# Kernel tuning notes

Measured on AMD Instinct MI355X. Metric: run time of the kernel, lower is better.

Reference implementation:

```python
import jax, jax.numpy as jnp
import numpy as np

B, T, F = 1024, 256, 64
H1, H2, H3 = 64, 32, 16


def _lstm_params(key, in_dim, units, scale=0.1):
    k1, k2, k3 = jax.random.split(key, 3)
    W = jax.random.normal(k1, (in_dim, 4 * units), jnp.float32) * scale
    U = jax.random.normal(k2, (units, 4 * units), jnp.float32) * scale
    b = jax.random.normal(k3, (4 * units,), jnp.float32) * scale
    return W, U, b


def lstm_seq(x, W, U, b, reverse):
    """Keras-style LSTM (gate order i,f,g,o). Returns (all_h [B,T,H] time-aligned, last_h [B,H])."""
    Bx = x.shape[0]
    H = U.shape[0]
    xz = jnp.einsum('bti,ij->btj', x, W) + b  # [B,T,4H]
    if reverse:
        xz = xz[:, ::-1]
    xz = jnp.swapaxes(xz, 0, 1)  # [T,B,4H]

    def step(carry, zx):
        h, c = carry
        z = zx + h @ U
        i, f, g, o = jnp.split(z, 4, axis=-1)
        i = jax.nn.sigmoid(i)
        f = jax.nn.sigmoid(f)
        g = jnp.tanh(g)
        o = jax.nn.sigmoid(o)
        c = f * c + i * g
        h = o * jnp.tanh(c)
        return (h, c), h

    h0 = jnp.zeros((Bx, H), x.dtype)
    (hT, _), hs = jax.lax.scan(step, (h0, h0), xz)
    hs = jnp.swapaxes(hs, 0, 1)  # [B,T,H]
    if reverse:
        hs = hs[:, ::-1]  # Keras Bidirectional re-reverses backward outputs
    return hs, hT


def setup_inputs() -> dict:
    key = jax.random.key(0)
    ks = jax.random.split(key, 10)
    x = jax.random.normal(ks[0], (B, T, F), jnp.float32)
    W1f, U1f, b1f = _lstm_params(ks[1], F, H1)
    W1b, U1b, b1b = _lstm_params(ks[2], F, H1)
    W2f, U2f, b2f = _lstm_params(ks[3], 2 * H1, H2)
    W2b, U2b, b2b = _lstm_params(ks[4], 2 * H1, H2)
    W3f, U3f, b3f = _lstm_params(ks[5], 2 * H2, H3)
    W3b, U3b, b3b = _lstm_params(ks[6], 2 * H2, H3)
    Wd1 = jax.random.normal(ks[7], (2 * H3, 16), jnp.float32) * 0.1
    bd1 = jnp.zeros((16,), jnp.float32)
    Wd2 = jax.random.normal(ks[8], (16, 2), jnp.float32) * 0.1
    bd2 = jnp.zeros((2,), jnp.float32)
    return dict(inputs=x,
                W1f=W1f, U1f=U1f, b1f=b1f, W1b=W1b, U1b=U1b, b1b=b1b,
                W2f=W2f, U2f=U2f, b2f=b2f, W2b=W2b, U2b=U2b, b2b=b2b,
                W3f=W3f, U3f=U3f, b3f=b3f, W3b=W3b, U3b=U3b, b3b=b3b,
                Wd1=Wd1, bd1=bd1, Wd2=Wd2, bd2=bd2)


def reference(inputs,
              W1f, U1f, b1f, W1b, U1b, b1b,
              W2f, U2f, b2f, W2b, U2b, b2b,
              W3f, U3f, b3f, W3b, U3b, b3b,
              Wd1, bd1, Wd2, bd2):
    # inference path: all dropout / GaussianDropout layers are identity
    hf, _ = lstm_seq(inputs, W1f, U1f, b1f, reverse=False)
    hb, _ = lstm_seq(inputs, W1b, U1b, b1b, reverse=True)
    x = jnp.concatenate([hf, hb], axis=-1)  # [B,T,128]

    hf, _ = lstm_seq(x, W2f, U2f, b2f, reverse=False)
    hb, _ = lstm_seq(x, W2b, U2b, b2b, reverse=True)
    x = jnp.concatenate([hf, hb], axis=-1)  # [B,T,64]

    _, hf_last = lstm_seq(x, W3f, U3f, b3f, reverse=False)
    _, hb_last = lstm_seq(x, W3b, U3b, b3b, reverse=True)
    x = jnp.concatenate([hf_last, hb_last], axis=-1)  # [B,32] (Flatten is identity)

    x = jnp.clip(x @ Wd1 + bd1, 0.0, 6.0)  # relu6
    logits = x @ Wd2 + bd2
    return jax.nn.softmax(logits, axis=-1)
```

## Files before the change

kernel.cpp:

```cpp
#include <hip/hip_runtime.h>
#include <hip/hip_bf16.h>

#define T_SEQ 256
#define BATCH 1024

typedef __attribute__((ext_vector_type(8))) short  short8;
typedef __attribute__((ext_vector_type(4))) float  floatx4;
typedef unsigned short ushort_t;
typedef unsigned int   uint_t;

template <int P> struct IC { static constexpr int v = P; };

constexpr float NL2E = -1.4426950408889634f;
constexpr float L2E2 =  2.8853900817779268f;

__device__ __forceinline__ float exp2_fast(float x) {
    float r; asm("v_exp_f32 %0, %1" : "=v"(r) : "v"(x)); return r;
}
__device__ __forceinline__ float rcp_fast(float x) {
    float r; asm("v_rcp_f32 %0, %1" : "=v"(r) : "v"(x)); return r;
}
__device__ __forceinline__ ushort_t f2bf(float f) {
    union { float f; uint_t u; } v; v.f = f;
    uint_t r = v.u + 0x7FFFu + ((v.u >> 16) & 1u);
    return (ushort_t)(r >> 16);
}
__device__ __forceinline__ uint_t pk_bf16(float a, float b) {
    union { __hip_bfloat162 h; uint_t u; } v;
    v.h = __float22bfloat162_rn(make_float2(a, b));
    return v.u;
}
__device__ __forceinline__ void sync_lds() {
    asm volatile("s_waitcnt lgkmcnt(0)\n\ts_barrier" ::: "memory");
}

template <int D, int H, bool IS_FIRST, bool SEQ_OUT>
__global__ __launch_bounds__(64 * (H / 16), 1) void lstm_fused(
    const void* __restrict__ xin,
    const float* __restrict__ Wf, const float* __restrict__ Uf, const float* __restrict__ bgf,
    const float* __restrict__ Wb, const float* __restrict__ Ub, const float* __restrict__ bgb,
    void* __restrict__ outp)
{
    constexpr int UG  = H / 16;
    constexpr int KSx = D / 32;
    constexpr int KSh = (H + 31) / 32;
    constexpr int KS  = KSx + KSh;
    constexpr int HP  = (H < 32 ? 32 : H) + 8;
    constexpr int G4  = 4 * H;
    constexpr int NTH = 64 * UG;
    static_assert(D % 32 == 0 && T_SEQ % 4 == 0, "shape");

    const int tid  = threadIdx.x;
    const int ug   = tid >> 6;
    const int lane = tid & 63;
    const int lm   = lane & 15;
    const int lq   = lane >> 4;
    const int dir  = blockIdx.y;
    const int b0   = blockIdx.x * 16;

    const float* W  = dir ? Wb  : Wf;
    const float* U  = dir ? Ub  : Uf;
    const float* bg = dir ? bgb : bgf;

    __shared__ __align__(16) ushort_t hbuf[2][16][HP];

    short8 bw[4][KS];
    float  bb[4];
#pragma unroll
    for (int g = 0; g < 4; g++) {
        const float sc = (g == 2) ? L2E2 : NL2E;
        const int n = g * H + ug * 16 + lm;
        bb[g] = sc * bg[n];
#pragma unroll
        for (int ks = 0; ks < KS; ks++) {
            short8 f;
#pragma unroll
            for (int e = 0; e < 8; e++) {
                const int k = ks * 32 + lq * 8 + e;
                float v = 0.0f;
                if (k < D)          v = W[k * G4 + n];
                else if (k < D + H) v = U[(k - D) * G4 + n];
                f[e] = (short)f2bf(sc * v);
            }
            bw[g][ks] = f;
        }
    }

    for (int idx = tid; idx < 2 * 16 * HP; idx += NTH)
        ((ushort_t*)hbuf)[idx] = 0;

    float cst[4] = {0.f, 0.f, 0.f, 0.f};
    float hl[4]  = {0.f, 0.f, 0.f, 0.f};

    const int t0 = dir ? T_SEQ - 1 : 0;
    const float*    pxf = (const float*)xin + ((size_t)(b0 + lm) * T_SEQ + t0) * D + lq * 8;
    const ushort_t* pxb = (const ushort_t*)xin + ((size_t)t0 * BATCH + b0 + lm) * D + lq * 8;
    const long xstepf = dir ? -(long)D : (long)D;
    const long xstepb = (dir ? -(long)BATCH : (long)BATCH) * D;
    ushort_t* pout = (ushort_t*)outp +
        ((size_t)t0 * BATCH + b0 + lq * 4) * (2 * H) + dir * H + ug * 16 + lm;
    const long ostep = (dir ? -(long)BATCH : (long)BATCH) * (2 * H);

    float4 rawf[4][2 * KSx];
    short8 rawb[4][KSx];

    auto load_slot = [&](auto sl_) {
        constexpr int SL = decltype(sl_)::v;
        if (IS_FIRST) {
#pragma unroll
            for (int ks = 0; ks < KSx; ks++) {
                rawf[SL][2 * ks + 0] = *(const float4*)(pxf + ks * 32 + 0);
                rawf[SL][2 * ks + 1] = *(const float4*)(pxf + ks * 32 + 4);
            }
            pxf += xstepf;
        } else {
#pragma unroll
            for (int ks = 0; ks < KSx; ks++)
                rawb[SL][ks] = *(const short8*)(pxb + ks * 32);
            pxb += xstepb;
        }
    };

    load_slot(IC<0>{}); load_slot(IC<1>{}); load_slot(IC<2>{}); load_slot(IC<3>{});
    __syncthreads();

    auto step = [&](auto p_, auto sl_, int s) {
        constexpr int P  = decltype(p_)::v;
        constexpr int SL = decltype(sl_)::v;

        short8 fh[KSh];
#pragma unroll
        for (int ks = 0; ks < KSh; ks++)
            fh[ks] = *(const short8*)&hbuf[P][lm][ks * 32 + lq * 8];

        floatx4 acc[4];
#pragma unroll
        for (int g = 0; g < 4; g++) acc[g] = (floatx4){bb[g], bb[g], bb[g], bb[g]};

        short8 av[KSx];
        if (IS_FIRST) {
#pragma unroll
            for (int ks = 0; ks < KSx; ks++) {
                union { short8 s; uint_t u[4]; } f;
                const float* ra = (const float*)&rawf[SL][2 * ks];
#pragma unroll
                for (int e = 0; e < 4; e++) f.u[e] = pk_bf16(ra[2 * e], ra[2 * e + 1]);
                av[ks] = f.s;
            }
        } else {
#pragma unroll
            for (int ks = 0; ks < KSx; ks++) av[ks] = rawb[SL][ks];
        }

#pragma unroll
        for (int ks = 0; ks < KSx; ks++)
#pragma unroll
            for (int g = 0; g < 4; g++)
                acc[g] = __builtin_amdgcn_mfma_f32_16x16x32_bf16(av[ks], bw[g][ks], acc[g], 0, 0, 0);

        if (s + 4 < T_SEQ) load_slot(sl_);

#pragma unroll
        for (int ks = 0; ks < KSh; ks++)
#pragma unroll
            for (int g = 0; g < 4; g++)
                acc[g] = __builtin_amdgcn_mfma_f32_16x16x32_bf16(fh[ks], bw[g][KSx + ks], acc[g], 0, 0, 0);

#pragma unroll
        for (int r = 0; r < 4; r++) {
            const float gi = rcp_fast(1.0f + exp2_fast(acc[0][r]));
            const float gf = rcp_fast(1.0f + exp2_fast(acc[1][r]));
            const float gg = 1.0f - 2.0f * rcp_fast(1.0f + exp2_fast(acc[2][r]));
            const float go = rcp_fast(1.0f + exp2_fast(acc[3][r]));
            cst[r] = fmaf(gf, cst[r], gi * gg);
            const float tc = 1.0f - 2.0f * rcp_fast(1.0f + exp2_fast(L2E2 * cst[r]));
            const float h = go * tc;
            hl[r] = h;
            const ushort_t hw = f2bf(h);
            hbuf[P ^ 1][lq * 4 + r][ug * 16 + lm] = hw;
            if (SEQ_OUT) pout[r * 2 * H] = hw;
        }
        pout += ostep;
        if (UG > 1) sync_lds();
    };

    for (int s = 0; s < T_SEQ; s += 4) {
        step(IC<0>{}, IC<0>{}, s);
        step(IC<1>{}, IC<1>{}, s + 1);
        step(IC<0>{}, IC<2>{}, s + 2);
        step(IC<1>{}, IC<3>{}, s + 3);
    }

    if (!SEQ_OUT) {
        float* op = (float*)outp;
#pragma unroll
        for (int r = 0; r < 4; r++)
            op[(size_t)(b0 + lq * 4 + r) * (2 * H) + dir * H + ug * 16 + lm] = hl[r];
    }
}

__global__ __launch_bounds__(256) void dense_head(
    const float* __restrict__ h3, const float* __restrict__ Wd1, const float* __restrict__ bd1,
    const float* __restrict__ Wd2, const float* __restrict__ bd2, float* __restrict__ out)
{
    const int b = blockIdx.x * blockDim.x + threadIdx.x;
    if (b >= BATCH) return;
    float x[32];
#pragma unroll
    for (int k = 0; k < 32; k++) x[k] = h3[b * 32 + k];
    float y[16];
#pragma unroll
    for (int jj = 0; jj < 16; jj++) {
        float a = bd1[jj];
#pragma unroll
        for (int k = 0; k < 32; k++) a = fmaf(x[k], Wd1[k * 16 + jj], a);
        y[jj] = fminf(fmaxf(a, 0.0f), 6.0f);
    }
    float l0 = bd2[0], l1 = bd2[1];
#pragma unroll
    for (int k = 0; k < 16; k++) {
        l0 = fmaf(y[k], Wd2[k * 2 + 0], l0);
        l1 = fmaf(y[k], Wd2[k * 2 + 1], l1);
    }
    const float m = fmaxf(l0, l1);
    const float e0 = __expf(l0 - m), e1 = __expf(l1 - m);
    const float inv = 1.0f / (e0 + e1);
    out[b * 2 + 0] = e0 * inv;
    out[b * 2 + 1] = e1 * inv;
}

extern "C" void kernel_launch(void* const* d_in, const int* in_sizes, int n_in,
                              void* d_out, int out_size, void* d_ws, size_t ws_size,
                              hipStream_t stream)
{
    const float* x   = (const float*)d_in[0];
    const float* W1f = (const float*)d_in[1];
    const float* U1f = (const float*)d_in[2];
    const float* b1f = (const float*)d_in[3];
    const float* W1b = (const float*)d_in[4];
    const float* U1b = (const float*)d_in[5];
    const float* b1b = (const float*)d_in[6];
    const float* W2f = (const float*)d_in[7];
    const float* U2f = (const float*)d_in[8];
    const float* b2f = (const float*)d_in[9];
    const float* W2b = (const float*)d_in[10];
    const float* U2b = (const float*)d_in[11];
    const float* b2b = (const float*)d_in[12];
    const float* W3f = (const float*)d_in[13];
    const float* U3f = (const float*)d_in[14];
    const float* b3f = (const float*)d_in[15];
    const float* W3b = (const float*)d_in[16];
    const float* U3b = (const float*)d_in[17];
    const float* b3b = (const float*)d_in[18];
    const float* Wd1 = (const float*)d_in[19];
    const float* bd1 = (const float*)d_in[20];
    const float* Wd2 = (const float*)d_in[21];
    const float* bd2 = (const float*)d_in[22];

    char* ws = (char*)d_ws;
    void*  l1out = (void*)ws;
    void*  l2out = (void*)(ws + (size_t)64 * 1024 * 1024);
    float* h3    = (float*)(ws + (size_t)96 * 1024 * 1024);
    float* out   = (float*)d_out;

    dim3 grid(BATCH / 16, 2);

    lstm_fused<64, 64, true, true>
        <<<grid, 256, 0, stream>>>(x, W1f, U1f, b1f, W1b, U1b, b1b, l1out);
    lstm_fused<128, 32, false, true>
        <<<grid, 128, 0, stream>>>(l1out, W2f, U2f, b2f, W2b, U2b, b2b, l2out);
    lstm_fused<64, 16, false, false>
        <<<grid, 64, 0, stream>>>(l2out, W3f, U3f, b3f, W3b, U3b, b3b, h3);
    dense_head<<<dim3(BATCH / 256), 256, 0, stream>>>(h3, Wd1, bd1, Wd2, bd2, out);
}
```

Measured before the change: 517.7 us.

## Transpose LSTM MFMA so hidden state stays in registers for small layers

Swaps the MFMA operand order so gate outputs come out batch-by-unit transposed, and each lane's output fragment matches the B-operand layout of a 16x16x16 MFMA. For layers 2 and 3 a single wave now computes all hidden units and feeds h back through registers, with no LDS round trip and no barrier per timestep. Output writes also become packed 8-byte stores, and the L2E2 scale is folded into the cell state. The cost is that one wave per block does the work of two for layer 2, which lengthens each step's serial MFMA chain and raises register pressure.

```diff
diff --git a/kernel.cpp b/kernel.cpp
--- a/kernel.cpp
+++ b/kernel.cpp
@@ -5,6 +5,7 @@
 #define BATCH 1024
 
 typedef __attribute__((ext_vector_type(8))) short  short8;
+typedef __attribute__((ext_vector_type(4))) short  short4v;
 typedef __attribute__((ext_vector_type(4))) float  floatx4;
 typedef unsigned short ushort_t;
 typedef unsigned int   uint_t;
@@ -33,18 +34,28 @@
 __device__ __forceinline__ void sync_lds() {
     asm volatile("s_waitcnt lgkmcnt(0)\n\ts_barrier" ::: "memory");
 }
-
-template <int D, int H, bool IS_FIRST, bool SEQ_OUT>
-__global__ __launch_bounds__(64 * (H / 16), 1) void lstm_fused(
+__device__ __forceinline__ floatx4 mfma16(short4v a, short4v b, floatx4 c) {
+#if __has_builtin(__builtin_amdgcn_mfma_f32_16x16x16bf16_1k)
+    return __builtin_amdgcn_mfma_f32_16x16x16bf16_1k(a, b, c, 0, 0, 0);
+#else
+    floatx4 d;
+    asm("v_mfma_f32_16x16x16_bf16 %0, %1, %2, %3" : "=v"(d) : "v"(a), "v"(b), "v"(c));
+    return d;
+#endif
+}
+
+template <int D, int H, bool IS_FIRST, bool SEQ_OUT, bool REGH>
+__global__ __launch_bounds__(REGH ? 64 : 64 * (H / 16), 1) void lstm_fused(
     const void* __restrict__ xin,
     const float* __restrict__ Wf, const float* __restrict__ Uf, const float* __restrict__ bgf,
     const float* __restrict__ Wb, const float* __restrict__ Ub, const float* __restrict__ bgb,
     void* __restrict__ outp)
 {
-    constexpr int UG  = H / 16;
+    constexpr int UG  = REGH ? 1 : H / 16;
+    constexpr int NT  = REGH ? H / 16 : 1;
     constexpr int KSx = D / 32;
-    constexpr int KSh = (H + 31) / 32;
-    constexpr int KS  = KSx + KSh;
+    constexpr int KSh = REGH ? 1 : H / 32;
+    constexpr int NC  = REGH ? H / 16 : 1;
     constexpr int HP  = (H < 32 ? 32 : H) + 8;
     constexpr int G4  = 4 * H;
     constexpr int NTH = 64 * UG;
@@ -62,35 +73,71 @@
     const float* U  = dir ? Ub  : Uf;
     const float* bg = dir ? bgb : bgf;
 
-    __shared__ __align__(16) ushort_t hbuf[2][16][HP];
-
-    short8 bw[4][KS];
-    float  bb[4];
+    __shared__ __align__(16) ushort_t hbuf[REGH ? 8 : 2 * 16 * HP];
+
+    short8  aw[4][NT][KSx];
+    short8  hw[4][NT][KSh];
+    short4v uw[4][NT][NC];
+    floatx4 bias4[4][NT];
 #pragma unroll
     for (int g = 0; g < 4; g++) {
         const float sc = (g == 2) ? L2E2 : NL2E;
-        const int n = g * H + ug * 16 + lm;
-        bb[g] = sc * bg[n];
-#pragma unroll
-        for (int ks = 0; ks < KS; ks++) {
-            short8 f;
-#pragma unroll
-            for (int e = 0; e < 8; e++) {
-                const int k = ks * 32 + lq * 8 + e;
-                float v = 0.0f;
-                if (k < D)          v = W[k * G4 + n];
-                else if (k < D + H) v = U[(k - D) * G4 + n];
-                f[e] = (short)f2bf(sc * v);
-            }
-            bw[g][ks] = f;
-        }
-    }
-
-    for (int idx = tid; idx < 2 * 16 * HP; idx += NTH)
-        ((ushort_t*)hbuf)[idx] = 0;
-
-    float cst[4] = {0.f, 0.f, 0.f, 0.f};
-    float hl[4]  = {0.f, 0.f, 0.f, 0.f};
+#pragma unroll
+        for (int t = 0; t < NT; t++) {
+            const int ub = g * H + (REGH ? t * 16 : ug * 16);
+            floatx4 b4;
+#pragma unroll
+            for (int r = 0; r < 4; r++) b4[r] = sc * bg[ub + lq * 4 + r];
+            bias4[g][t] = b4;
+            const int nc = ub + lm;
+#pragma unroll
+            for (int ks = 0; ks < KSx; ks++) {
+                short8 f;
+#pragma unroll
+                for (int e = 0; e < 8; e++)
+                    f[e] = (short)f2bf(sc * W[(ks * 32 + lq * 8 + e) * G4 + nc]);
+                aw[g][t][ks] = f;
+            }
+            if constexpr (!REGH) {
+#pragma unroll
+                for (int ks = 0; ks < KSh; ks++) {
+                    short8 f;
+#pragma unroll
+                    for (int e = 0; e < 8; e++) {
+                        const int k = ks * 32 + lq * 8 + e;
+                        f[e] = (k < H) ? (short)f2bf(sc * U[k * G4 + nc]) : (short)0;
+                    }
+                    hw[g][t][ks] = f;
+                }
+            } else {
+#pragma unroll
+                for (int c = 0; c < NC; c++) {
+                    short4v f;
+#pragma unroll
+                    for (int e = 0; e < 4; e++)
+                        f[e] = (short)f2bf(sc * U[(c * 16 + lq * 4 + e) * G4 + nc]);
+                    uw[g][t][c] = f;
+                }
+            }
+        }
+    }
+
+    if constexpr (!REGH) {
+        for (int idx = tid; idx < 2 * 16 * HP; idx += NTH)
+            hbuf[idx] = 0;
+    }
+
+    float   cst[NT][4];
+    float   hl[NT][4];
+    short4v hfrag[NC];
+#pragma unroll
+    for (int t = 0; t < NT; t++)
+#pragma unroll
+        for (int r = 0; r < 4; r++) { cst[t][r] = 0.f; hl[t][r] = 0.f; }
+    if constexpr (REGH) {
+#pragma unroll
+        for (int c = 0; c < NC; c++) hfrag[c] = (short4v){0, 0, 0, 0};
+    }
 
     const int t0 = dir ? T_SEQ - 1 : 0;
     const float*    pxf = (const float*)xin + ((size_t)(b0 + lm) * T_SEQ + t0) * D + lq * 8;
@@ -98,7 +145,7 @@
     const long xstepf = dir ? -(long)D : (long)D;
     const long xstepb = (dir ? -(long)BATCH : (long)BATCH) * D;
     ushort_t* pout = (ushort_t*)outp +
-        ((size_t)t0 * BATCH + b0 + lq * 4) * (2 * H) + dir * H + ug * 16 + lm;
+        ((size_t)t0 * BATCH + b0 + lm) * (2 * H) + dir * H + (REGH ? 0 : ug * 16) + lq * 4;
     const long ostep = (dir ? -(long)BATCH : (long)BATCH) * (2 * H);
 
     float4 rawf[4][2 * KSx];
@@ -122,20 +169,18 @@
     };
 
     load_slot(IC<0>{}); load_slot(IC<1>{}); load_slot(IC<2>{}); load_slot(IC<3>{});
-    __syncthreads();
+    if constexpr (!REGH) __syncthreads();
 
     auto step = [&](auto p_, auto sl_, int s) {
         constexpr int P  = decltype(p_)::v;
         constexpr int SL = decltype(sl_)::v;
 
         short8 fh[KSh];
-#pragma unroll
-        for (int ks = 0; ks < KSh; ks++)
-            fh[ks] = *(const short8*)&hbuf[P][lm][ks * 32 + lq * 8];
-
-        floatx4 acc[4];
-#pragma unroll
-        for (int g = 0; g < 4; g++) acc[g] = (floatx4){bb[g], bb[g], bb[g], bb[g]};
+        if constexpr (!REGH) {
+#pragma unroll
+            for (int ks = 0; ks < KSh; ks++)
+                fh[ks] = *(const short8*)&hbuf[(P * 16 + lm) * HP + ks * 32 + lq * 8];
+        }
 
         short8 av[KSx];
         if (IS_FIRST) {
@@ -152,33 +197,68 @@
             for (int ks = 0; ks < KSx; ks++) av[ks] = rawb[SL][ks];
         }
 
-#pragma unroll
-        for (int ks = 0; ks < KSx; ks++)
+        floatx4 acc[4][NT];
+#pragma unroll
+        for (int g = 0; g < 4; g++)
+#pragma unroll
+            for (int t = 0; t < NT; t++)
+                acc[g][t] = __builtin_amdgcn_mfma_f32_16x16x32_bf16(aw[g][t][0], av[0], bias4[g][t], 0, 0, 0);
+#pragma unroll
+        for (int ks = 1; ks < KSx; ks++)
 #pragma unroll
             for (int g = 0; g < 4; g++)
-                acc[g] = __builtin_amdgcn_mfma_f32_16x16x32_bf16(av[ks], bw[g][ks], acc[g], 0, 0, 0);
+#pragma unroll
+                for (int t = 0; t < NT; t++)
+                    acc[g][t] = __builtin_amdgcn_mfma_f32_16x16x32_bf16(aw[g][t][ks], av[ks], acc[g][t], 0, 0, 0);
 
         if (s + 4 < T_SEQ) load_slot(sl_);
 
-#pragma unroll
-        for (int ks = 0; ks < KSh; ks++)
-#pragma unroll
-            for (int g = 0; g < 4; g++)
-                acc[g] = __builtin_amdgcn_mfma_f32_16x16x32_bf16(fh[ks], bw[g][KSx + ks], acc[g], 0, 0, 0);
-
-#pragma unroll
-        for (int r = 0; r < 4; r++) {
-            const float gi = rcp_fast(1.0f + exp2_fast(acc[0][r]));
-            const float gf = rcp_fast(1.0f + exp2_fast(acc[1][r]));
-            const float gg = 1.0f - 2.0f * rcp_fast(1.0f + exp2_fast(acc[2][r]));
-            const float go = rcp_fast(1.0f + exp2_fast(acc[3][r]));
-            cst[r] = fmaf(gf, cst[r], gi * gg);
-            const float tc = 1.0f - 2.0f * rcp_fast(1.0f + exp2_fast(L2E2 * cst[r]));
-            const float h = go * tc;
-            hl[r] = h;
-            const ushort_t hw = f2bf(h);
-            hbuf[P ^ 1][lq * 4 + r][ug * 16 + lm] = hw;
-            if (SEQ_OUT) pout[r * 2 * H] = hw;
+        if constexpr (!REGH) {
+#pragma unroll
+            for (int ks = 0; ks < KSh; ks++)
+#pragma unroll
+                for (int g = 0; g < 4; g++)
+                    acc[g][0] = __builtin_amdgcn_mfma_f32_16x16x32_bf16(hw[g][0][ks], fh[ks], acc[g][0], 0, 0, 0);
+        } else {
+#pragma unroll
+            for (int c = 0; c < NC; c++)
+#pragma unroll
+                for (int g = 0; g < 4; g++)
+#pragma unroll
+                    for (int t = 0; t < NT; t++)
+                        acc[g][t] = mfma16(uw[g][t][c], hfrag[c], acc[g][t]);
+        }
+
+#pragma unroll
+        for (int t = 0; t < NT; t++) {
+            float hv[4];
+#pragma unroll
+            for (int r = 0; r < 4; r++) {
+                const float gi = rcp_fast(1.0f + exp2_fast(acc[0][t][r]));
+                const float gf = rcp_fast(1.0f + exp2_fast(acc[1][t][r]));
+                const float gg = 1.0f - 2.0f * rcp_fast(1.0f + exp2_fast(acc[2][t][r]));
+                const float go = rcp_fast(1.0f + exp2_fast(acc[3][t][r]));
+                cst[t][r] = fmaf(gf, cst[t][r], L2E2 * (gi * gg));
+                const float tc = 1.0f - 2.0f * rcp_fast(1.0f + exp2_fast(cst[t][r]));
+                hv[r] = go * tc;
+            }
+            const uint_t d0 = pk_bf16(hv[0], hv[1]);
+            const uint_t d1 = pk_bf16(hv[2], hv[3]);
+            if constexpr (REGH) {
+                union { uint_t u[2]; short4v s; } pp;
+                pp.u[0] = d0; pp.u[1] = d1;
+                hfrag[t] = pp.s;
+            } else {
+                uint2 wv; wv.x = d0; wv.y = d1;
+                *(uint2*)&hbuf[((P ^ 1) * 16 + lm) * HP + ug * 16 + lq * 4] = wv;
+            }
+            if (SEQ_OUT) {
+                uint2 ov; ov.x = d0; ov.y = d1;
+                *(uint2*)&pout[t * 16] = ov;
+            } else {
+#pragma unroll
+                for (int r = 0; r < 4; r++) hl[t][r] = hv[r];
+            }
         }
         pout += ostep;
         if (UG > 1) sync_lds();
@@ -194,8 +274,10 @@
     if (!SEQ_OUT) {
         float* op = (float*)outp;
 #pragma unroll
-        for (int r = 0; r < 4; r++)
-            op[(size_t)(b0 + lq * 4 + r) * (2 * H) + dir * H + ug * 16 + lm] = hl[r];
+        for (int t = 0; t < NT; t++) {
+            float4 v4 = make_float4(hl[t][0], hl[t][1], hl[t][2], hl[t][3]);
+            *(float4*)&op[(size_t)(b0 + lm) * (2 * H) + dir * H + (REGH ? t * 16 : ug * 16) + lq * 4] = v4;
+        }
     }
 }
 
@@ -265,11 +347,11 @@
 
     dim3 grid(BATCH / 16, 2);
 
-    lstm_fused<64, 64, true, true>
+    lstm_fused<64, 64, true, true, false>
         <<<grid, 256, 0, stream>>>(x, W1f, U1f, b1f, W1b, U1b, b1b, l1out);
-    lstm_fused<128, 32, false, true>
-        <<<grid, 128, 0, stream>>>(l1out, W2f, U2f, b2f, W2b, U2b, b2b, l2out);
-    lstm_fused<64, 16, false, false>
+    lstm_fused<128, 32, false, true, true>
+        <<<grid, 64, 0, stream>>>(l1out, W2f, U2f, b2f, W2b, U2b, b2b, l2out);
+    lstm_fused<64, 16, false, false, true>
         <<<grid, 64, 0, stream>>>(l2out, W3f, U3f, b3f, W3b, U3b, b3b, h3);
     dense_head<<<dim3(BATCH / 256), 256, 0, stream>>>(h3, Wd1, bd1, Wd2, bd2, out);
 }
```

Measured after the change: 641.5 us. 23.9% more time.

## Batch gate reciprocals and swap MFMA operands for vectorized h stores in layers 2-3

Applied to the files above, without the earlier changes.

Gate nonlinearities are now evaluated four at a time with a shared reciprocal (a product trick that needs one rcp per four sigmoids), which cuts transcendental instructions on the serial recurrence path. For layers 2 and 3, the MFMA operands are swapped so each lane holds four consecutive hidden units of one batch row, which allows packed 8-byte LDS and global stores of h instead of four scalar 2-byte stores. The bias is folded into the first MFMA as the accumulator input. The shared-reciprocal product of four (1+exp) terms can overflow to inf when gate pre-activations are large, which risks NaN or zero outputs.

```diff
diff --git a/kernel.cpp b/kernel.cpp
--- a/kernel.cpp
+++ b/kernel.cpp
@@ -34,17 +34,36 @@
     asm volatile("s_waitcnt lgkmcnt(0)\n\ts_barrier" ::: "memory");
 }
 
-template <int D, int H, bool IS_FIRST, bool SEQ_OUT>
+
+__device__ __forceinline__ void sig4(const float z[4], float o[4]) {
+    const float A0 = 1.0f + exp2_fast(z[0]);
+    const float A1 = 1.0f + exp2_fast(z[1]);
+    const float A2 = 1.0f + exp2_fast(z[2]);
+    const float A3 = 1.0f + exp2_fast(z[3]);
+    const float P01 = A0 * A1, P23 = A2 * A3;
+    const float R   = rcp_fast(P01 * P23);
+    const float R01 = R * P23;
+    const float R23 = R * P01;
+    o[0] = R01 * A1; o[1] = R01 * A0;
+    o[2] = R23 * A3; o[3] = R23 * A2;
+}
+__device__ __forceinline__ void tanh4(const float z[4], float o[4]) {
+    float s[4]; sig4(z, s);
+#pragma unroll
+    for (int r = 0; r < 4; r++) o[r] = fmaf(-2.0f, s[r], 1.0f);
+}
+
+template <int D, int H, bool IS_FIRST, bool SEQ_OUT, int MODE>
 __global__ __launch_bounds__(64 * (H / 16), 1) void lstm_fused(
     const void* __restrict__ xin,
     const float* __restrict__ Wf, const float* __restrict__ Uf, const float* __restrict__ bgf,
     const float* __restrict__ Wb, const float* __restrict__ Ub, const float* __restrict__ bgb,
     void* __restrict__ outp)
 {
+    constexpr bool SW = (MODE >= 1);
     constexpr int UG  = H / 16;
     constexpr int KSx = D / 32;
     constexpr int KSh = (H + 31) / 32;
-    constexpr int KS  = KSx + KSh;
     constexpr int HP  = (H < 32 ? 32 : H) + 8;
     constexpr int G4  = 4 * H;
     constexpr int NTH = 64 * UG;
@@ -62,43 +81,61 @@
     const float* U  = dir ? Ub  : Uf;
     const float* bg = dir ? bgb : bgf;
 
-    __shared__ __align__(16) ushort_t hbuf[2][16][HP];
-
-    short8 bw[4][KS];
-    float  bb[4];
+    __shared__ __align__(16) ushort_t hbuf[2 * 16 * HP];
+
+    short8  aw[4][KSx];
+    short8  hw[4][KSh];
+    floatx4 bias4[4];
 #pragma unroll
     for (int g = 0; g < 4; g++) {
         const float sc = (g == 2) ? L2E2 : NL2E;
-        const int n = g * H + ug * 16 + lm;
-        bb[g] = sc * bg[n];
-#pragma unroll
-        for (int ks = 0; ks < KS; ks++) {
+        const int ub = g * H + ug * 16;
+        floatx4 b4;
+#pragma unroll
+        for (int r = 0; r < 4; r++)
+            b4[r] = sc * bg[ub + (SW ? lq * 4 + r : lm)];
+        bias4[g] = b4;
+        const int nc = ub + lm;
+#pragma unroll
+        for (int ks = 0; ks < KSx; ks++) {
+            short8 f;
+#pragma unroll
+            for (int e = 0; e < 8; e++)
+                f[e] = (short)f2bf(sc * W[(ks * 32 + lq * 8 + e) * G4 + nc]);
+            aw[g][ks] = f;
+        }
+#pragma unroll
+        for (int ks = 0; ks < KSh; ks++) {
             short8 f;
 #pragma unroll
             for (int e = 0; e < 8; e++) {
                 const int k = ks * 32 + lq * 8 + e;
-                float v = 0.0f;
-                if (k < D)          v = W[k * G4 + n];
-                else if (k < D + H) v = U[(k - D) * G4 + n];
-                f[e] = (short)f2bf(sc * v);
-            }
-            bw[g][ks] = f;
+                f[e] = (k < H) ? (short)f2bf(sc * U[k * G4 + nc]) : (short)0;
+            }
+            hw[g][ks] = f;
         }
     }
 
     for (int idx = tid; idx < 2 * 16 * HP; idx += NTH)
-        ((ushort_t*)hbuf)[idx] = 0;
-
-    float cst[4] = {0.f, 0.f, 0.f, 0.f};
-    float hl[4]  = {0.f, 0.f, 0.f, 0.f};
+        hbuf[idx] = 0;
+
+    float cst[4];
+    float hl[4];
+#pragma unroll
+    for (int r = 0; r < 4; r++) { cst[r] = 0.f; hl[r] = 0.f; }
 
     const int t0 = dir ? T_SEQ - 1 : 0;
     const float*    pxf = (const float*)xin + ((size_t)(b0 + lm) * T_SEQ + t0) * D + lq * 8;
     const ushort_t* pxb = (const ushort_t*)xin + ((size_t)t0 * BATCH + b0 + lm) * D + lq * 8;
     const long xstepf = dir ? -(long)D : (long)D;
     const long xstepb = (dir ? -(long)BATCH : (long)BATCH) * D;
-    ushort_t* pout = (ushort_t*)outp +
-        ((size_t)t0 * BATCH + b0 + lq * 4) * (2 * H) + dir * H + ug * 16 + lm;
+    ushort_t* pout;
+    if constexpr (SW)
+        pout = (ushort_t*)outp + ((size_t)t0 * BATCH + b0 + lm) * (2 * H) + dir * H +
+               ug * 16 + lq * 4;
+    else
+        pout = (ushort_t*)outp + ((size_t)t0 * BATCH + b0 + lq * 4) * (2 * H) + dir * H +
+               ug * 16 + lm;
     const long ostep = (dir ? -(long)BATCH : (long)BATCH) * (2 * H);
 
     float4 rawf[4][2 * KSx];
@@ -131,11 +168,7 @@
         short8 fh[KSh];
 #pragma unroll
         for (int ks = 0; ks < KSh; ks++)
-            fh[ks] = *(const short8*)&hbuf[P][lm][ks * 32 + lq * 8];
-
-        floatx4 acc[4];
-#pragma unroll
-        for (int g = 0; g < 4; g++) acc[g] = (floatx4){bb[g], bb[g], bb[g], bb[g]};
+            fh[ks] = *(const short8*)&hbuf[(P * 16 + lm) * HP + ks * 32 + lq * 8];
 
         short8 av[KSx];
         if (IS_FIRST) {
@@ -152,11 +185,19 @@
             for (int ks = 0; ks < KSx; ks++) av[ks] = rawb[SL][ks];
         }
 
-#pragma unroll
-        for (int ks = 0; ks < KSx; ks++)
+        floatx4 acc[4];
+#pragma unroll
+        for (int g = 0; g < 4; g++)
+            acc[g] = SW
+                ? __builtin_amdgcn_mfma_f32_16x16x32_bf16(aw[g][0], av[0], bias4[g], 0, 0, 0)
+                : __builtin_amdgcn_mfma_f32_16x16x32_bf16(av[0], aw[g][0], bias4[g], 0, 0, 0);
+#pragma unroll
+        for (int ks = 1; ks < KSx; ks++)
 #pragma unroll
             for (int g = 0; g < 4; g++)
-                acc[g] = __builtin_amdgcn_mfma_f32_16x16x32_bf16(av[ks], bw[g][ks], acc[g], 0, 0, 0);
+                acc[g] = SW
+                    ? __builtin_amdgcn_mfma_f32_16x16x32_bf16(aw[g][ks], av[ks], acc[g], 0, 0, 0)
+                    : __builtin_amdgcn_mfma_f32_16x16x32_bf16(av[ks], aw[g][ks], acc[g], 0, 0, 0);
 
         if (s + 4 < T_SEQ) load_slot(sl_);
 
@@ -164,21 +205,50 @@
         for (int ks = 0; ks < KSh; ks++)
 #pragma unroll
             for (int g = 0; g < 4; g++)
-                acc[g] = __builtin_amdgcn_mfma_f32_16x16x32_bf16(fh[ks], bw[g][KSx + ks], acc[g], 0, 0, 0);
-
+                acc[g] = SW
+                    ? __builtin_amdgcn_mfma_f32_16x16x32_bf16(hw[g][ks], fh[ks], acc[g], 0, 0, 0)
+                    : __builtin_amdgcn_mfma_f32_16x16x32_bf16(fh[ks], hw[g][ks], acc[g], 0, 0, 0);
+
+        float zi[4], zf[4], zg[4], zo[4];
 #pragma unroll
         for (int r = 0; r < 4; r++) {
-            const float gi = rcp_fast(1.0f + exp2_fast(acc[0][r]));
-            const float gf = rcp_fast(1.0f + exp2_fast(acc[1][r]));
-            const float gg = 1.0f - 2.0f * rcp_fast(1.0f + exp2_fast(acc[2][r]));
-            const float go = rcp_fast(1.0f + exp2_fast(acc[3][r]));
-            cst[r] = fmaf(gf, cst[r], gi * gg);
-            const float tc = 1.0f - 2.0f * rcp_fast(1.0f + exp2_fast(L2E2 * cst[r]));
-            const float h = go * tc;
-            hl[r] = h;
-            const ushort_t hw = f2bf(h);
-            hbuf[P ^ 1][lq * 4 + r][ug * 16 + lm] = hw;
-            if (SEQ_OUT) pout[r * 2 * H] = hw;
+            zi[r] = acc[0][r]; zf[r] = acc[1][r];
+            zg[r] = acc[2][r]; zo[r] = acc[3][r];
+        }
+        float gi[4], gf[4], gg[4], go[4];
+        sig4(zi, gi); sig4(zf, gf); tanh4(zg, gg); sig4(zo, go);
+        float cz[4];
+#pragma unroll
+        for (int r = 0; r < 4; r++) {
+            cst[r] = fmaf(gf[r], cst[r], L2E2 * (gi[r] * gg[r]));
+            cz[r] = cst[r];
+        }
+        float tc[4];
+        tanh4(cz, tc);
+        float hv[4];
+#pragma unroll
+        for (int r = 0; r < 4; r++) hv[r] = go[r] * tc[r];
+
+        if constexpr (SW) {
+            const uint_t d0 = pk_bf16(hv[0], hv[1]);
+            const uint_t d1 = pk_bf16(hv[2], hv[3]);
+            uint2 wv; wv.x = d0; wv.y = d1;
+            *(uint2*)&hbuf[((P ^ 1) * 16 + lm) * HP + ug * 16 + lq * 4] = wv;
+            if (SEQ_OUT) {
+                uint2 ov; ov.x = d0; ov.y = d1;
+                *(uint2*)&pout[0] = ov;
+            } else {
+#pragma unroll
+                for (int r = 0; r < 4; r++) hl[r] = hv[r];
+            }
+        } else {
+#pragma unroll
+            for (int r = 0; r < 4; r++) {
+                const ushort_t hw_ = f2bf(hv[r]);
+                hbuf[((P ^ 1) * 16 + lq * 4 + r) * HP + ug * 16 + lm] = hw_;
+                if (SEQ_OUT) pout[r * 2 * H] = hw_;
+                else         hl[r] = hv[r];
+            }
         }
         pout += ostep;
         if (UG > 1) sync_lds();
@@ -193,9 +263,14 @@
 
     if (!SEQ_OUT) {
         float* op = (float*)outp;
-#pragma unroll
-        for (int r = 0; r < 4; r++)
-            op[(size_t)(b0 + lq * 4 + r) * (2 * H) + dir * H + ug * 16 + lm] = hl[r];
+        if constexpr (SW) {
+            float4 v4 = make_float4(hl[0], hl[1], hl[2], hl[3]);
+            *(float4*)&op[(size_t)(b0 + lm) * (2 * H) + dir * H + ug * 16 + lq * 4] = v4;
+        } else {
+#pragma unroll
+            for (int r = 0; r < 4; r++)
+                op[(size_t)(b0 + lq * 4 + r) * (2 * H) + dir * H + ug * 16 + lm] = hl[r];
+        }
     }
 }
 
@@ -265,11 +340,11 @@
 
     dim3 grid(BATCH / 16, 2);
 
-    lstm_fused<64, 64, true, true>
+    lstm_fused<64, 64, true, true, 0>
         <<<grid, 256, 0, stream>>>(x, W1f, U1f, b1f, W1b, U1b, b1b, l1out);
-    lstm_fused<128, 32, false, true>
+    lstm_fused<128, 32, false, true, 1>
         <<<grid, 128, 0, stream>>>(l1out, W2f, U2f, b2f, W2b, U2b, b2b, l2out);
-    lstm_fused<64, 16, false, false>
+    lstm_fused<64, 16, false, false, 1>
         <<<grid, 64, 0, stream>>>(l2out, W3f, U3f, b3f, W3b, U3b, b3b, h3);
     dense_head<<<dim3(BATCH / 256), 256, 0, stream>>>(h3, Wd1, bd1, Wd2, bd2, out);
 }
```

After: 497.4 us (median of 2 runs). 3.9% less time.
